# Kernel tuning notes

Hardware: AMD Instinct MI355X
Metric: run time of the kernel (lower is better)

## Reference

```python
import jax, jax.numpy as jnp
import numpy as np

B, S, D_IN = 4, 2048, 1024
H, D_HEAD = 16, 64  # per-head output dim d_output=64


def setup_inputs() -> dict:
    key = jax.random.key(0)
    ks = jax.random.split(key, 9)
    s_in = 1.0 / np.sqrt(D_IN)
    s_o = 1.0 / np.sqrt(H * D_HEAD)
    return {
        "x": jax.random.normal(ks[0], (B, S, D_IN), dtype=jnp.float32),
        "Wq": jax.random.uniform(ks[1], (H, D_IN, D_HEAD), jnp.float32, -s_in, s_in),
        "bq": jax.random.uniform(ks[2], (H, D_HEAD), jnp.float32, -s_in, s_in),
        "Wk": jax.random.uniform(ks[3], (H, D_IN, D_HEAD), jnp.float32, -s_in, s_in),
        "bk": jax.random.uniform(ks[4], (H, D_HEAD), jnp.float32, -s_in, s_in),
        "Wv": jax.random.uniform(ks[5], (H, D_IN, D_HEAD), jnp.float32, -s_in, s_in),
        "bv": jax.random.uniform(ks[6], (H, D_HEAD), jnp.float32, -s_in, s_in),
        "Wo": jax.random.uniform(ks[7], (H * D_HEAD, D_HEAD), jnp.float32, -s_o, s_o),
        "bo": jax.random.uniform(ks[8], (D_HEAD,), jnp.float32, -s_o, s_o),
    }


def reference(x, Wq, bq, Wk, bk, Wv, bv, Wo, bo):
    # per-head projections: [B,H,S,Dh]
    q = jnp.einsum("bsd,hde->bhse", x, Wq) + bq[None, :, None, :]
    k = jnp.einsum("bsd,hde->bhse", x, Wk) + bk[None, :, None, :]
    v = jnp.einsum("bsd,hde->bhse", x, Wv) + bv[None, :, None, :]
    scale = 1.0 / np.sqrt(D_HEAD)
    scores = jnp.einsum("bhqe,bhke->bhqk", q, k) * scale  # [B,H,S,S]
    seq_len = x.shape[1]
    causal = jnp.tril(jnp.ones((seq_len, seq_len), dtype=bool))
    scores = jnp.where(causal[None, None], scores, -jnp.inf)
    attn = jax.nn.softmax(scores, axis=-1)  # dropout=0 -> identity
    out = jnp.einsum("bhqk,bhke->bhqe", attn, v)  # [B,H,S,Dh]
    # concat heads along feature dim (head order matches torch cat)
    out = out.transpose(0, 2, 1, 3).reshape(x.shape[0], seq_len, H * D_HEAD)
    return out @ Wo + bo
```

## Files before the change

kernel.cpp:

```cpp
#include <hip/hip_runtime.h>

typedef unsigned short u16;
typedef unsigned int u32;
typedef __attribute__((ext_vector_type(8))) short s16x8;
typedef __attribute__((ext_vector_type(4))) float f32x4;

#define MFMA(a,b,c) __builtin_amdgcn_mfma_f32_16x16x32_bf16((a),(b),(c),0,0,0)
#define QSCALE 0.18033688011112042f

#define BAR() do { asm volatile("" ::: "memory"); __builtin_amdgcn_s_barrier(); asm volatile("" ::: "memory"); } while(0)
#define WAITV(n) asm volatile("s_waitcnt vmcnt(" #n ")" ::: "memory")

__device__ __forceinline__ u16 bfc(float f){
  union { float f; unsigned int u; } c; c.f = f;
  return (u16)((c.u + 0x7fffu + ((c.u >> 16) & 1u)) >> 16);
}
__device__ __forceinline__ u32 pkbf(float lo, float hi){
  union { float f; u32 u; } a, b; a.f = lo; b.f = hi;
  return __builtin_amdgcn_perm(b.u + 0x8000u, a.u + 0x8000u, 0x07060302u);
}
__device__ __forceinline__ float fexp2(float x){ return __builtin_amdgcn_exp2f(x); }
__device__ __forceinline__ f32x4 zero4(){ f32x4 z; z[0]=0.f; z[1]=0.f; z[2]=0.f; z[3]=0.f; return z; }

__device__ __forceinline__ void gload_lds16(const u16* g, u16* l){
  __builtin_amdgcn_global_load_lds((const __attribute__((address_space(1))) unsigned int*)g,
                                   (__attribute__((address_space(3))) unsigned int*)l, 16, 0, 0);
}

__global__ __launch_bounds__(256) void k_prep(const float* __restrict__ x,
    const float* __restrict__ Wq, const float* __restrict__ Wk,
    const float* __restrict__ Wv, const float* __restrict__ Wo,
    u16* __restrict__ xb, u16* __restrict__ wt, u16* __restrict__ wot){
  __shared__ float t[64][65];
  int tid = threadIdx.x;
  if (blockIdx.x < 2048){
    int base = blockIdx.x * 256 + tid;
    #pragma unroll
    for (int j = 0; j < 4; j++){
      int i = (base + j * 524288) * 4;
      float4 v = *(const float4*)(x + i);
      *(uint2*)(xb + i) = make_uint2(pkbf(v.x, v.y), pkbf(v.z, v.w));
    }
    return;
  }
  int tt = blockIdx.x - 2048;
  int k0 = (tt & 15) * 64, y = tt >> 4;
  const float* src; u16* dst;
  if (y < 16)      { src = Wq + (size_t)y * 65536;        dst = wt + (size_t)y * 65536; }
  else if (y < 32) { src = Wk + (size_t)(y-16) * 65536;   dst = wt + (size_t)y * 65536; }
  else if (y < 48) { src = Wv + (size_t)(y-32) * 65536;   dst = wt + (size_t)y * 65536; }
  else             { src = Wo;                            dst = wot; }
  const float* s = src + (size_t)k0 * 64;
  int kl = tid >> 2, nc = (tid & 3) * 16;
  #pragma unroll
  for (int j = 0; j < 4; j++){
    float4 v = *(const float4*)(s + kl * 64 + nc + j * 4);
    t[kl][nc + j*4 + 0] = v.x; t[kl][nc + j*4 + 1] = v.y;
    t[kl][nc + j*4 + 2] = v.z; t[kl][nc + j*4 + 3] = v.w;
  }
  __syncthreads();
  int n = tid >> 2, kc = (tid & 3) * 16;
  u16 o[16];
  #pragma unroll
  for (int j = 0; j < 16; j++) o[j] = bfc(t[kc + j][n]);
  u16* d = dst + (size_t)n * 1024 + k0 + kc;
  *(uint4*)(d)     = *(uint4*)&o[0];
  *(uint4*)(d + 8) = *(uint4*)&o[8];
}

__global__ __launch_bounds__(256) void k_qkv(const u16* __restrict__ xb, const u16* __restrict__ wt,
    const float* __restrict__ bq, const float* __restrict__ bk, const float* __restrict__ bv,
    u16* __restrict__ Qo, u16* __restrict__ Ko, u16* __restrict__ VT){
  __shared__ u16 lds[24576];
  int tid = threadIdx.x, w = tid >> 6, lane = tid & 63;
  int l16 = lane & 15, g = lane >> 4;
  int row0 = blockIdx.x * 128, col0 = blockIdx.y * 128;
  int wm = (w & 1) * 64, wn = (w >> 1) * 64;
  f32x4 acc[4][4];
  #pragma unroll
  for (int mt = 0; mt < 4; mt++)
    #pragma unroll
    for (int nt = 0; nt < 4; nt++) acc[mt][nt] = zero4();

  int trow = tid >> 2;
  int lc = (tid & 3) ^ ((tid >> 3) & 3);
  const u16* gpa = xb + (size_t)(row0 + trow) * 1024 + lc * 8;
  const u16* gpb = wt + (size_t)(col0 + trow) * 1024 + lc * 8;

  int afo[4], bfo[4];
  #pragma unroll
  for (int mt = 0; mt < 4; mt++){
    int r = wm + mt * 16 + l16;
    afo[mt] = r * 32 + ((g ^ ((r >> 1) & 3)) * 8);
  }
  #pragma unroll
  for (int nt = 0; nt < 4; nt++){
    int r = wn + nt * 16 + l16;
    bfo[nt] = 4096 + r * 32 + ((g ^ ((r >> 1) & 3)) * 8);
  }

  auto stage = [&](int sl, int slot){
    u16* base = &lds[slot * 8192 + w * 512];
    int ko = sl * 32;
    gload_lds16(gpa + ko,             base);
    gload_lds16(gpa + ko + 64 * 1024, base + 2048);
    gload_lds16(gpb + ko,             base + 4096);
    gload_lds16(gpb + ko + 64 * 1024, base + 4096 + 2048);
  };
  auto compute = [&](int sel){
    s16x8 af[4], bf[4];
    #pragma unroll
    for (int mt = 0; mt < 4; mt++) af[mt] = *(const s16x8*)&lds[sel + afo[mt]];
    #pragma unroll
    for (int nt = 0; nt < 4; nt++) bf[nt] = *(const s16x8*)&lds[sel + bfo[nt]];
    __builtin_amdgcn_s_setprio(1);
    #pragma unroll
    for (int mt = 0; mt < 4; mt++)
      #pragma unroll
      for (int nt = 0; nt < 4; nt++) acc[mt][nt] = MFMA(af[mt], bf[nt], acc[mt][nt]);
    __builtin_amdgcn_s_setprio(0);
  };

  stage(0, 0); stage(1, 1);
  #pragma unroll 3
  for (int s = 0; s < 30; ++s){
    WAITV(4);
    BAR();
    stage(s + 2, (s + 2) % 3);
    compute((s % 3) * 8192);
  }
  WAITV(0); BAR();
  compute(0);
  compute(8192);

  #pragma unroll
  for (int nt = 0; nt < 4; nt++){
    int n = col0 + wn + nt * 16 + l16;
    int wi = n >> 10, hh = (n >> 6) & 15, dh = n & 63;
    const float* bptr = (wi == 0) ? bq : (wi == 1) ? bk : bv;
    float bval = bptr[hh * 64 + dh];
    #pragma unroll
    for (int mt = 0; mt < 4; mt++){
      int m0 = row0 + wm + mt * 16 + g * 4;
      int bb = m0 >> 11, ss = m0 & 2047;
      if (wi == 2){
        u32 p0 = pkbf(acc[mt][nt][0] + bval, acc[mt][nt][1] + bval);
        u32 p1 = pkbf(acc[mt][nt][2] + bval, acc[mt][nt][3] + bval);
        *(uint2*)&VT[(((size_t)bb * 16 + hh) * 64 + dh) * 2048 + ss] = make_uint2(p0, p1);
      } else {
        u16* dst = (wi == 0) ? Qo : Ko;
        float scl = (wi == 0) ? QSCALE : 1.0f;
        #pragma unroll
        for (int i = 0; i < 4; i++)
          dst[(((size_t)bb * 16 + hh) * 2048 + ss + i) * 64 + dh] = bfc((acc[mt][nt][i] + bval) * scl);
      }
    }
  }
}

__global__ __launch_bounds__(256, 3) void k_attn(const u16* __restrict__ Q, const u16* __restrict__ Kg,
    const u16* __restrict__ VT, u16* __restrict__ O){
  __shared__ u16 smem[18432];
  u16* Ks = smem;
  u16* Vt = smem + 4608;
  u16* Ps = smem + 9216;
  int hbi = blockIdx.x;
  int qt = 15 - (int)blockIdx.y;
  int b = hbi >> 4, h = hbi & 15;
  int tid = threadIdx.x, wave = tid >> 6, lane = tid & 63;
  int l16 = lane & 15, g = lane >> 4;
  size_t hb = (size_t)hbi * 2048 * 64;
  const u16* kbase = Kg + hb;
  const u16* vbase = VT + hb;
  int sr = tid >> 3, scc = (tid & 7) * 8;
  u16* PsW = Ps + wave * (32 * 72);
  int q0 = qt * 128 + wave * 32;
  s16x8 bq[2][2];
  #pragma unroll
  for (int j = 0; j < 2; j++)
    #pragma unroll
    for (int c = 0; c < 2; c++)
      bq[j][c] = *(const s16x8*)(Q + hb + (size_t)(q0 + j*16 + l16) * 64 + c*32 + g*8);
  f32x4 accO[4][2];
  #pragma unroll
  for (int mt = 0; mt < 4; mt++)
    #pragma unroll
    for (int j = 0; j < 2; j++) accO[mt][j] = zero4();
  float rs0 = 0.f, rs1 = 0.f;
  int nkt = 2 * qt + 2;
  uint4 ka0, ka1, va0, va1;
  ka0 = *(const uint4*)(kbase + (size_t)(sr)      * 64 + scc);
  ka1 = *(const uint4*)(kbase + (size_t)(sr + 32) * 64 + scc);
  va0 = *(const uint4*)(vbase + (size_t)(sr)      * 2048 + scc);
  va1 = *(const uint4*)(vbase + (size_t)(sr + 32) * 2048 + scc);
  *(uint4*)&Ks[sr * 72 + scc] = ka0; *(uint4*)&Ks[(sr + 32) * 72 + scc] = ka1;
  *(uint4*)&Vt[sr * 72 + scc] = va0; *(uint4*)&Vt[(sr + 32) * 72 + scc] = va1;
  __syncthreads();
  for (int kt = 0; kt < nkt; kt++){
    if (kt + 1 < nkt){
      int kb2 = (kt + 1) * 64;
      ka0 = *(const uint4*)(kbase + (size_t)(kb2 + sr)      * 64 + scc);
      ka1 = *(const uint4*)(kbase + (size_t)(kb2 + sr + 32) * 64 + scc);
      va0 = *(const uint4*)(vbase + (size_t)(sr)      * 2048 + kb2 + scc);
      va1 = *(const uint4*)(vbase + (size_t)(sr + 32) * 2048 + kb2 + scc);
    }
    int ks0 = kt * 64;
    if (ks0 <= q0 + 31){
      #pragma unroll
      for (int kb = 0; kb < 4; kb++){
        s16x8 ak0 = *(const s16x8*)&Ks[(kb*16 + l16) * 72 + g*8];
        s16x8 ak1 = *(const s16x8*)&Ks[(kb*16 + l16) * 72 + 32 + g*8];
        #pragma unroll
        for (int j = 0; j < 2; j++){
          f32x4 s = zero4();
          s = MFMA(ak0, bq[j][0], s);
          s = MFMA(ak1, bq[j][1], s);
          if (ks0 + kb*16 + 15 > q0 + j*16){
            int qrow = q0 + j*16 + l16;
            #pragma unroll
            for (int r = 0; r < 4; r++)
              if (ks0 + kb*16 + g*4 + r > qrow) s[r] = -1e30f;
          }
          float p0 = fexp2(s[0]), p1 = fexp2(s[1]), p2 = fexp2(s[2]), p3 = fexp2(s[3]);
          if (j == 0) rs0 += (p0 + p1) + (p2 + p3);
          else        rs1 += (p0 + p1) + (p2 + p3);
          *(uint2*)&PsW[(j*16 + l16) * 72 + kb*16 + g*4] = make_uint2(pkbf(p0, p1), pkbf(p2, p3));
        }
      }
      s16x8 av[4][2];
      #pragma unroll
      for (int mt = 0; mt < 4; mt++)
        #pragma unroll
        for (int kc = 0; kc < 2; kc++)
          av[mt][kc] = *(const s16x8*)&Vt[(mt*16 + l16) * 72 + kc*32 + g*8];
      #pragma unroll
      for (int j = 0; j < 2; j++){
        s16x8 bp0 = *(const s16x8*)&PsW[(j*16 + l16) * 72 + g*8];
        s16x8 bp1 = *(const s16x8*)&PsW[(j*16 + l16) * 72 + 32 + g*8];
        #pragma unroll
        for (int mt = 0; mt < 4; mt++){
          accO[mt][j] = MFMA(av[mt][0], bp0, accO[mt][j]);
          accO[mt][j] = MFMA(av[mt][1], bp1, accO[mt][j]);
        }
      }
    }
    if (kt + 1 < nkt){
      __syncthreads();
      *(uint4*)&Ks[sr * 72 + scc] = ka0; *(uint4*)&Ks[(sr + 32) * 72 + scc] = ka1;
      *(uint4*)&Vt[sr * 72 + scc] = va0; *(uint4*)&Vt[(sr + 32) * 72 + scc] = va1;
      __syncthreads();
    }
  }
  float rinv[2];
  #pragma unroll
  for (int j = 0; j < 2; j++){
    float l = (j == 0) ? rs0 : rs1;
    l += __shfl_xor(l, 16);
    l += __shfl_xor(l, 32);
    rinv[j] = 1.0f / l;
  }
  #pragma unroll
  for (int mt = 0; mt < 4; mt++)
    #pragma unroll
    for (int j = 0; j < 2; j++){
      float o0 = accO[mt][j][0] * rinv[j];
      float o1 = accO[mt][j][1] * rinv[j];
      float o2 = accO[mt][j][2] * rinv[j];
      float o3 = accO[mt][j][3] * rinv[j];
      *(uint2*)&O[((size_t)b * 2048 + q0 + j*16 + l16) * 1024 + h*64 + mt*16 + g*4] =
          make_uint2(pkbf(o0, o1), pkbf(o2, o3));
    }
}

__global__ __launch_bounds__(256) void k_oproj(const u16* __restrict__ Ob, const u16* __restrict__ wot,
    const float* __restrict__ bo, float* __restrict__ out){
  __shared__ u16 As[64][72];
  __shared__ u16 Bs[64][72];
  int rb = blockIdx.x;
  int tid = threadIdx.x, wave = tid >> 6, lane = tid & 63;
  int l16 = lane & 15, g = lane >> 4;
  int wr = (wave & 1) * 32, wc = (wave >> 1) * 32;
  int row0 = rb * 64;
  f32x4 acc[2][2];
  acc[0][0]=zero4(); acc[0][1]=zero4(); acc[1][0]=zero4(); acc[1][1]=zero4();
  int r0s = tid >> 3, cc0 = (tid & 7) * 8, r1s = r0s + 32;
  for (int k0 = 0; k0 < 1024; k0 += 64){
    __syncthreads();
    *(uint4*)&As[r0s][cc0] = *(const uint4*)(Ob + (size_t)(row0 + r0s) * 1024 + k0 + cc0);
    *(uint4*)&As[r1s][cc0] = *(const uint4*)(Ob + (size_t)(row0 + r1s) * 1024 + k0 + cc0);
    *(uint4*)&Bs[r0s][cc0] = *(const uint4*)(wot + (size_t)r0s * 1024 + k0 + cc0);
    *(uint4*)&Bs[r1s][cc0] = *(const uint4*)(wot + (size_t)r1s * 1024 + k0 + cc0);
    __syncthreads();
    #pragma unroll
    for (int c = 0; c < 2; c++){
      int kcc = c * 32;
      s16x8 a0 = *(const s16x8*)&As[wr      + l16][kcc + g * 8];
      s16x8 a1 = *(const s16x8*)&As[wr + 16 + l16][kcc + g * 8];
      s16x8 b0 = *(const s16x8*)&Bs[wc      + l16][kcc + g * 8];
      s16x8 b1 = *(const s16x8*)&Bs[wc + 16 + l16][kcc + g * 8];
      acc[0][0] = MFMA(a0, b0, acc[0][0]);
      acc[0][1] = MFMA(a0, b1, acc[0][1]);
      acc[1][0] = MFMA(a1, b0, acc[1][0]);
      acc[1][1] = MFMA(a1, b1, acc[1][1]);
    }
  }
  #pragma unroll
  for (int rt = 0; rt < 2; rt++){
    #pragma unroll
    for (int ct = 0; ct < 2; ct++){
      int col = wc + ct * 16 + l16;
      float bval = bo[col];
      #pragma unroll
      for (int i = 0; i < 4; i++){
        int row = row0 + wr + rt * 16 + g * 4 + i;
        out[(size_t)row * 64 + col] = acc[rt][ct][i] + bval;
      }
    }
  }
}

extern "C" void kernel_launch(void* const* d_in, const int* in_sizes, int n_in,
                              void* d_out, int out_size, void* d_ws, size_t ws_size,
                              hipStream_t stream){
  const float* x  = (const float*)d_in[0];
  const float* Wq = (const float*)d_in[1];
  const float* bq = (const float*)d_in[2];
  const float* Wk = (const float*)d_in[3];
  const float* bk = (const float*)d_in[4];
  const float* Wv = (const float*)d_in[5];
  const float* bv = (const float*)d_in[6];
  const float* Wo = (const float*)d_in[7];
  const float* bo = (const float*)d_in[8];

  u16* xb  = (u16*)d_ws;
  u16* wt  = xb  + 8388608;
  u16* wot = wt  + 3145728;
  u16* Qb  = wot + 65536;
  u16* Kb  = Qb  + 8388608;
  u16* VTb = Kb  + 8388608;
  u16* Ob  = xb;
  float* out = (float*)d_out;

  k_prep<<<2832, 256, 0, stream>>>(x, Wq, Wk, Wv, Wo, xb, wt, wot);
  k_qkv<<<dim3(64, 24), 256, 0, stream>>>(xb, wt, bq, bk, bv, Qb, Kb, VTb);
  k_attn<<<dim3(64, 16), 256, 0, stream>>>(Qb, Kb, VTb, Ob);
  k_oproj<<<128, 256, 0, stream>>>(Ob, wot, bo, out);
}
```

Baseline: 239.2 us.

## Load K/V directly from global in attention and halve oproj row tile

The attention kernel stops staging K and V^T tiles in shared memory with block-wide barriers. Each wave now reads its MFMA operands straight from global memory and loops only over the key tiles it needs for causal masking. This removes the two __syncthreads per tile and lets waves run independently, but every wave re-reads the same K/V data through cache with no explicit prefetch. Separately, the output projection uses 32-row blocks with a 256-block grid to spread work over more CUs.

```diff
diff --git a/kernel.cpp b/kernel.cpp
--- a/kernel.cpp
+++ b/kernel.cpp
@@ -160,10 +160,7 @@
 
 __global__ __launch_bounds__(256, 3) void k_attn(const u16* __restrict__ Q, const u16* __restrict__ Kg,
     const u16* __restrict__ VT, u16* __restrict__ O){
-  __shared__ u16 smem[18432];
-  u16* Ks = smem;
-  u16* Vt = smem + 4608;
-  u16* Ps = smem + 9216;
+  __shared__ u16 Ps[4 * 32 * 72];
   int hbi = blockIdx.x;
   int qt = 15 - (int)blockIdx.y;
   int b = hbi >> 4, h = hbi & 15;
@@ -172,7 +169,6 @@
   size_t hb = (size_t)hbi * 2048 * 64;
   const u16* kbase = Kg + hb;
   const u16* vbase = VT + hb;
-  int sr = tid >> 3, scc = (tid & 7) * 8;
   u16* PsW = Ps + wave * (32 * 72);
   int q0 = qt * 128 + wave * 32;
   s16x8 bq[2][2];
@@ -187,68 +183,46 @@
     #pragma unroll
     for (int j = 0; j < 2; j++) accO[mt][j] = zero4();
   float rs0 = 0.f, rs1 = 0.f;
-  int nkt = 2 * qt + 2;
-  uint4 ka0, ka1, va0, va1;
-  ka0 = *(const uint4*)(kbase + (size_t)(sr)      * 64 + scc);
-  ka1 = *(const uint4*)(kbase + (size_t)(sr + 32) * 64 + scc);
-  va0 = *(const uint4*)(vbase + (size_t)(sr)      * 2048 + scc);
-  va1 = *(const uint4*)(vbase + (size_t)(sr + 32) * 2048 + scc);
-  *(uint4*)&Ks[sr * 72 + scc] = ka0; *(uint4*)&Ks[(sr + 32) * 72 + scc] = ka1;
-  *(uint4*)&Vt[sr * 72 + scc] = va0; *(uint4*)&Vt[(sr + 32) * 72 + scc] = va1;
-  __syncthreads();
-  for (int kt = 0; kt < nkt; kt++){
-    if (kt + 1 < nkt){
-      int kb2 = (kt + 1) * 64;
-      ka0 = *(const uint4*)(kbase + (size_t)(kb2 + sr)      * 64 + scc);
-      ka1 = *(const uint4*)(kbase + (size_t)(kb2 + sr + 32) * 64 + scc);
-      va0 = *(const uint4*)(vbase + (size_t)(sr)      * 2048 + kb2 + scc);
-      va1 = *(const uint4*)(vbase + (size_t)(sr + 32) * 2048 + kb2 + scc);
-    }
+  int myNkt = ((q0 + 31) >> 6) + 1;
+  for (int kt = 0; kt < myNkt; kt++){
     int ks0 = kt * 64;
-    if (ks0 <= q0 + 31){
-      #pragma unroll
-      for (int kb = 0; kb < 4; kb++){
-        s16x8 ak0 = *(const s16x8*)&Ks[(kb*16 + l16) * 72 + g*8];
-        s16x8 ak1 = *(const s16x8*)&Ks[(kb*16 + l16) * 72 + 32 + g*8];
-        #pragma unroll
-        for (int j = 0; j < 2; j++){
-          f32x4 s = zero4();
-          s = MFMA(ak0, bq[j][0], s);
-          s = MFMA(ak1, bq[j][1], s);
-          if (ks0 + kb*16 + 15 > q0 + j*16){
-            int qrow = q0 + j*16 + l16;
-            #pragma unroll
-            for (int r = 0; r < 4; r++)
-              if (ks0 + kb*16 + g*4 + r > qrow) s[r] = -1e30f;
-          }
-          float p0 = fexp2(s[0]), p1 = fexp2(s[1]), p2 = fexp2(s[2]), p3 = fexp2(s[3]);
-          if (j == 0) rs0 += (p0 + p1) + (p2 + p3);
-          else        rs1 += (p0 + p1) + (p2 + p3);
-          *(uint2*)&PsW[(j*16 + l16) * 72 + kb*16 + g*4] = make_uint2(pkbf(p0, p1), pkbf(p2, p3));
-        }
-      }
-      s16x8 av[4][2];
-      #pragma unroll
-      for (int mt = 0; mt < 4; mt++)
-        #pragma unroll
-        for (int kc = 0; kc < 2; kc++)
-          av[mt][kc] = *(const s16x8*)&Vt[(mt*16 + l16) * 72 + kc*32 + g*8];
+    #pragma unroll
+    for (int kb = 0; kb < 4; kb++){
+      const u16* krow = kbase + (size_t)(ks0 + kb*16 + l16) * 64 + g*8;
+      s16x8 ak0 = *(const s16x8*)(krow);
+      s16x8 ak1 = *(const s16x8*)(krow + 32);
       #pragma unroll
       for (int j = 0; j < 2; j++){
-        s16x8 bp0 = *(const s16x8*)&PsW[(j*16 + l16) * 72 + g*8];
-        s16x8 bp1 = *(const s16x8*)&PsW[(j*16 + l16) * 72 + 32 + g*8];
-        #pragma unroll
-        for (int mt = 0; mt < 4; mt++){
-          accO[mt][j] = MFMA(av[mt][0], bp0, accO[mt][j]);
-          accO[mt][j] = MFMA(av[mt][1], bp1, accO[mt][j]);
+        f32x4 s = zero4();
+        s = MFMA(ak0, bq[j][0], s);
+        s = MFMA(ak1, bq[j][1], s);
+        if (ks0 + kb*16 + 15 > q0 + j*16){
+          int qrow = q0 + j*16 + l16;
+          #pragma unroll
+          for (int r = 0; r < 4; r++)
+            if (ks0 + kb*16 + g*4 + r > qrow) s[r] = -1e30f;
         }
+        float p0 = fexp2(s[0]), p1 = fexp2(s[1]), p2 = fexp2(s[2]), p3 = fexp2(s[3]);
+        if (j == 0) rs0 += (p0 + p1) + (p2 + p3);
+        else        rs1 += (p0 + p1) + (p2 + p3);
+        *(uint2*)&PsW[(j*16 + l16) * 72 + kb*16 + g*4] = make_uint2(pkbf(p0, p1), pkbf(p2, p3));
       }
     }
-    if (kt + 1 < nkt){
-      __syncthreads();
-      *(uint4*)&Ks[sr * 72 + scc] = ka0; *(uint4*)&Ks[(sr + 32) * 72 + scc] = ka1;
-      *(uint4*)&Vt[sr * 72 + scc] = va0; *(uint4*)&Vt[(sr + 32) * 72 + scc] = va1;
-      __syncthreads();
+    s16x8 av[4][2];
+    #pragma unroll
+    for (int mt = 0; mt < 4; mt++)
+      #pragma unroll
+      for (int kc = 0; kc < 2; kc++)
+        av[mt][kc] = *(const s16x8*)(vbase + (size_t)(mt*16 + l16) * 2048 + ks0 + kc*32 + g*8);
+    #pragma unroll
+    for (int j = 0; j < 2; j++){
+      s16x8 bp0 = *(const s16x8*)&PsW[(j*16 + l16) * 72 + g*8];
+      s16x8 bp1 = *(const s16x8*)&PsW[(j*16 + l16) * 72 + 32 + g*8];
+      #pragma unroll
+      for (int mt = 0; mt < 4; mt++){
+        accO[mt][j] = MFMA(av[mt][0], bp0, accO[mt][j]);
+        accO[mt][j] = MFMA(av[mt][1], bp1, accO[mt][j]);
+      }
     }
   }
   float rinv[2];
@@ -274,49 +248,38 @@
 
 __global__ __launch_bounds__(256) void k_oproj(const u16* __restrict__ Ob, const u16* __restrict__ wot,
     const float* __restrict__ bo, float* __restrict__ out){
-  __shared__ u16 As[64][72];
+  __shared__ u16 As[32][72];
   __shared__ u16 Bs[64][72];
   int rb = blockIdx.x;
-  int tid = threadIdx.x, wave = tid >> 6, lane = tid & 63;
+  int tid = threadIdx.x, w = tid >> 6, lane = tid & 63;
   int l16 = lane & 15, g = lane >> 4;
-  int wr = (wave & 1) * 32, wc = (wave >> 1) * 32;
-  int row0 = rb * 64;
-  f32x4 acc[2][2];
-  acc[0][0]=zero4(); acc[0][1]=zero4(); acc[1][0]=zero4(); acc[1][1]=zero4();
-  int r0s = tid >> 3, cc0 = (tid & 7) * 8, r1s = r0s + 32;
+  int row0 = rb * 32;
+  f32x4 acc[2];
+  acc[0] = zero4(); acc[1] = zero4();
+  int ar = tid >> 3, cc0 = (tid & 7) * 8;
+  int br = tid >> 3;
   for (int k0 = 0; k0 < 1024; k0 += 64){
     __syncthreads();
-    *(uint4*)&As[r0s][cc0] = *(const uint4*)(Ob + (size_t)(row0 + r0s) * 1024 + k0 + cc0);
-    *(uint4*)&As[r1s][cc0] = *(const uint4*)(Ob + (size_t)(row0 + r1s) * 1024 + k0 + cc0);
-    *(uint4*)&Bs[r0s][cc0] = *(const uint4*)(wot + (size_t)r0s * 1024 + k0 + cc0);
-    *(uint4*)&Bs[r1s][cc0] = *(const uint4*)(wot + (size_t)r1s * 1024 + k0 + cc0);
+    *(uint4*)&As[ar][cc0]      = *(const uint4*)(Ob  + (size_t)(row0 + ar) * 1024 + k0 + cc0);
+    *(uint4*)&Bs[br][cc0]      = *(const uint4*)(wot + (size_t)br * 1024 + k0 + cc0);
+    *(uint4*)&Bs[br + 32][cc0] = *(const uint4*)(wot + (size_t)(br + 32) * 1024 + k0 + cc0);
     __syncthreads();
     #pragma unroll
     for (int c = 0; c < 2; c++){
-      int kcc = c * 32;
-      s16x8 a0 = *(const s16x8*)&As[wr      + l16][kcc + g * 8];
-      s16x8 a1 = *(const s16x8*)&As[wr + 16 + l16][kcc + g * 8];
-      s16x8 b0 = *(const s16x8*)&Bs[wc      + l16][kcc + g * 8];
-      s16x8 b1 = *(const s16x8*)&Bs[wc + 16 + l16][kcc + g * 8];
-      acc[0][0] = MFMA(a0, b0, acc[0][0]);
-      acc[0][1] = MFMA(a0, b1, acc[0][1]);
-      acc[1][0] = MFMA(a1, b0, acc[1][0]);
-      acc[1][1] = MFMA(a1, b1, acc[1][1]);
-    }
-  }
-  #pragma unroll
-  for (int rt = 0; rt < 2; rt++){
-    #pragma unroll
-    for (int ct = 0; ct < 2; ct++){
-      int col = wc + ct * 16 + l16;
-      float bval = bo[col];
-      #pragma unroll
-      for (int i = 0; i < 4; i++){
-        int row = row0 + wr + rt * 16 + g * 4 + i;
-        out[(size_t)row * 64 + col] = acc[rt][ct][i] + bval;
-      }
-    }
-  }
+      s16x8 a0 = *(const s16x8*)&As[l16][c*32 + g*8];
+      s16x8 a1 = *(const s16x8*)&As[16 + l16][c*32 + g*8];
+      s16x8 b  = *(const s16x8*)&Bs[w*16 + l16][c*32 + g*8];
+      acc[0] = MFMA(a0, b, acc[0]);
+      acc[1] = MFMA(a1, b, acc[1]);
+    }
+  }
+  int col = w * 16 + l16;
+  float bval = bo[col];
+  #pragma unroll
+  for (int rt = 0; rt < 2; rt++)
+    #pragma unroll
+    for (int i = 0; i < 4; i++)
+      out[(size_t)(row0 + rt*16 + g*4 + i) * 64 + col] = acc[rt][i] + bval;
 }
 
 extern "C" void kernel_launch(void* const* d_in, const int* in_sizes, int n_in,
@@ -344,5 +307,5 @@
   k_prep<<<2832, 256, 0, stream>>>(x, Wq, Wk, Wv, Wo, xb, wt, wot);
   k_qkv<<<dim3(64, 24), 256, 0, stream>>>(xb, wt, bq, bk, bv, Qb, Kb, VTb);
   k_attn<<<dim3(64, 16), 256, 0, stream>>>(Qb, Kb, VTb, Ob);
-  k_oproj<<<128, 256, 0, stream>>>(Ob, wot, bo, out);
-}
+  k_oproj<<<256, 256, 0, stream>>>(Ob, wot, bo, out);
+}
```

Result: slower. 309.0 us (+29.2%).
